# Performance work log

Measured on AMD Instinct MI355X. Metric: run time of the kernel, lower is better.

## Reference

```python
import jax, jax.numpy as jnp
import numpy as np

EPS = 1e-6      # F.pairwise_distance adds eps to the difference vector
MARGIN = 0.2
NORM_EPS = 1e-12  # torch F.normalize clamps the norm at 1e-12


def _l2_normalize(x):
    n = jnp.linalg.norm(x, axis=1, keepdims=True)
    return x / jnp.maximum(n, NORM_EPS)


def _pairdist(A, B):
    # ||a - b + EPS||_2 for every (a, b) pair, computed without the [N,N,d] tensor:
    # ||a-b||^2 + 2*EPS*sum(a-b) + d*EPS^2
    d = A.shape[1]
    sq = (jnp.sum(A * A, axis=1)[:, None] + jnp.sum(B * B, axis=1)[None, :]
          - 2.0 * (A @ B.T)
          + 2.0 * EPS * (jnp.sum(A, axis=1)[:, None] - jnp.sum(B, axis=1)[None, :])
          + d * (EPS * EPS))
    return jnp.sqrt(jnp.maximum(sq, 0.0))


def setup_inputs() -> dict:
    key = jax.random.key(0)
    kp, kn = jax.random.split(key)
    p = jax.random.normal(kp, (8192, 128), dtype=jnp.float32)
    n = jax.random.normal(kn, (64, 128), dtype=jnp.float32)
    return {"sequence_representations_p": p, "sequence_representations_n": n}


def reference(sequence_representations_p, sequence_representations_n):
    p = _l2_normalize(sequence_representations_p)  # [l_p, d]
    n = _l2_normalize(sequence_representations_n)  # [l_n, d]
    l_p = p.shape[0]
    t = 0  # original uses random.randint(0, l_n-1); fixed for determinism
    d_pp = _pairdist(p, p)                 # [l_p, l_p]
    d_pn = _pairdist(p, n[t:t + 1])[:, 0]  # [l_p]
    distance = jnp.maximum(d_pp + MARGIN - d_pn[:, None], 0.0)
    loss = jnp.sum(distance) / ((l_p - 1) * l_p)
    return jnp.maximum(loss, 0.0)
```

## Files before the change

kernel.cpp:

```cpp
#include <hip/hip_runtime.h>
#include <hip/hip_bf16.h>

typedef float f32x16 __attribute__((ext_vector_type(16)));
typedef float f32x4v __attribute__((ext_vector_type(4)));

#define GLOBAL_AS(p) ((const __attribute__((address_space(1))) void*)(p))
#define LDS_AS(p)    ((__attribute__((address_space(3))) void*)(p))

#define LP 8192
#define D 128
#define TWOEPS 2e-6f
#define CEPS 1.28e-10f
#define MARGIN 0.2f
#define NTRI 2080
#define NBLK 512
#define INV_DENOM 1.4903545e-8f

#define BUFSZ 34816
#define AOFF 0
#define BOFF 16384
#define QWOFF 32768

__global__ __launch_bounds__(64) void rows_kernel(const float* __restrict__ p,
                                                  const float* __restrict__ n,
                                                  char* __restrict__ pb,
                                                  float* __restrict__ qw) {
    const int lane = threadIdx.x;
    const int sub = lane & 3;
    const int r = lane >> 2;
    const int row = blockIdx.x * 16 + r;

    const float4* px = (const float4*)(p + (size_t)row * D + sub * 32);
    const float4* nx = (const float4*)(n + sub * 32);
    float4 x[8], y[8];
#pragma unroll
    for (int k = 0; k < 8; ++k) { x[k] = px[k]; y[k] = nx[k]; }

    float ssp = 0.0f, ssn = 0.0f;
#pragma unroll
    for (int k = 0; k < 8; ++k) {
        ssp += fmaf(x[k].x, x[k].x, fmaf(x[k].y, x[k].y,
               fmaf(x[k].z, x[k].z, x[k].w * x[k].w)));
        ssn += fmaf(y[k].x, y[k].x, fmaf(y[k].y, y[k].y,
               fmaf(y[k].z, y[k].z, y[k].w * y[k].w)));
    }
    ssp += __shfl_xor(ssp, 1); ssp += __shfl_xor(ssp, 2);
    ssn += __shfl_xor(ssn, 1); ssn += __shfl_xor(ssn, 2);

    const float invp = 1.0f / fmaxf(sqrtf(ssp), 1e-12f);
    const float invn = 1.0f / fmaxf(sqrtf(ssn), 1e-12f);

    float s = 0.0f, q = 0.0f, dn = 0.0f, sn = 0.0f, qn = 0.0f, q8 = 0.0f;
    int pk8[8];
#pragma unroll
    for (int k = 0; k < 8; ++k) {
        float a0 = x[k].x * invp, a1 = x[k].y * invp,
              a2 = x[k].z * invp, a3 = x[k].w * invp;
        float h0 = y[k].x * invn, h1 = y[k].y * invn,
              h2 = y[k].z * invn, h3 = y[k].w * invn;
        s  += (a0 + a1) + (a2 + a3);
        q  += fmaf(a0, a0, fmaf(a1, a1, fmaf(a2, a2, a3 * a3)));
        dn += fmaf(a0, h0, fmaf(a1, h1, fmaf(a2, h2, a3 * h3)));
        sn += (h0 + h1) + (h2 + h3);
        qn += fmaf(h0, h0, fmaf(h1, h1, fmaf(h2, h2, h3 * h3)));
        int wlo = __builtin_amdgcn_cvt_pk_fp8_f32(a0, a1, 0, false);
        int wfl = __builtin_amdgcn_cvt_pk_fp8_f32(a2, a3, wlo, true);
        pk8[k] = wfl;
        float b0 = __builtin_amdgcn_cvt_f32_fp8(wfl, 0);
        float b1 = __builtin_amdgcn_cvt_f32_fp8(wfl, 1);
        float b2 = __builtin_amdgcn_cvt_f32_fp8(wfl, 2);
        float b3 = __builtin_amdgcn_cvt_f32_fp8(wfl, 3);
        q8 += fmaf(b0, b0, fmaf(b1, b1, fmaf(b2, b2, b3 * b3)));
    }
    char* dst = pb + (size_t)row * 128 + sub * 32;
    ((int4*)dst)[0] = make_int4(pk8[0], pk8[1], pk8[2], pk8[3]);
    ((int4*)dst)[1] = make_int4(pk8[4], pk8[5], pk8[6], pk8[7]);

#pragma unroll
    for (int m = 1; m < 4; m <<= 1) {
        s += __shfl_xor(s, m);
        q += __shfl_xor(q, m);
        dn += __shfl_xor(dn, m);
        sn += __shfl_xor(sn, m);
        qn += __shfl_xor(qn, m);
        q8 += __shfl_xor(q8, m);
    }
    if (sub == 0) {
        float sq = q + qn - 2.0f * dn + TWOEPS * (s - sn) + CEPS;
        float dpn = sqrtf(fmaxf(sq, 0.0f));
        *(float2*)(qw + (size_t)row * 2) = make_float2(q8, MARGIN - dpn);
    }
}

__global__ __launch_bounds__(512, 4) void pair_kernel(const char* __restrict__ pb,
                                                      const float* __restrict__ qw,
                                                      float* __restrict__ out) {
    __shared__ __align__(16) char smem[2 * BUFSZ];
    const int blk = blockIdx.x;
    const int tid = threadIdx.x;
    const int wave = tid >> 6, lane = tid & 63;
    const int nt = (blk < NTRI - 4 * NBLK) ? 5 : 4;

    const int wr = wave >> 2, wc = wave & 3;
    const int ln31 = lane & 31;
    const int h = lane >> 5;

    auto decode = [](int b, int& ti, int& tj) {
        int t = (int)((__builtin_amdgcn_sqrtf(8.0f * (float)b + 1.0f) - 1.0f) * 0.5f);
        while ((t + 1) * (t + 2) / 2 <= b) ++t;
        while (t * (t + 1) / 2 > b) --t;
        ti = t;
        tj = b - t * (t + 1) / 2;
    };

    auto stage = [&](int ti, int tj, char* buf) {
        const char* gA = pb + (size_t)ti * 128 * 128;
        const char* gB = pb + (size_t)tj * 128 * 128;
#pragma unroll
        for (int r = 0; r < 2; ++r) {
            int obase = wave * 2048 + r * 1024;
            int o = obase + lane * 16;
            int src = o ^ (((o >> 7) & 7) << 4);
            __builtin_amdgcn_global_load_lds(GLOBAL_AS(gA + src),
                                             LDS_AS(buf + AOFF + obase), 16, 0, 0);
            __builtin_amdgcn_global_load_lds(GLOBAL_AS(gB + src),
                                             LDS_AS(buf + BOFF + obase), 16, 0, 0);
        }
        int side = wave >> 2;
        int chunk = wave & 3;
        const char* gq = (const char*)qw + (size_t)(side ? tj : ti) * 1024 +
                         chunk * 256 + lane * 4;
        __builtin_amdgcn_global_load_lds(GLOBAL_AS(gq),
                                         LDS_AS(buf + QWOFF + side * 1024 + chunk * 256),
                                         4, 0, 0);
    };

    int ti0, tj0;
    decode(blk, ti0, tj0);
    stage(ti0, tj0, smem);
    bool diag_cur = (ti0 == tj0);
    bool diag_nxt = false;

    float la0 = 0.0f, la1 = 0.0f, lb0 = 0.0f, lb1 = 0.0f;

    for (int t = 0; t < nt; ++t) {
        char* cur = smem + (size_t)(t & 1) * BUFSZ;
        char* nxt = smem + (size_t)((t + 1) & 1) * BUFSZ;

        if (t + 1 < nt) {
            int ti, tj;
            decode(blk + (t + 1) * NBLK, ti, tj);
            diag_nxt = (ti == tj);
            stage(ti, tj, nxt);
            asm volatile("s_waitcnt vmcnt(5)" ::: "memory");
        } else {
            asm volatile("s_waitcnt vmcnt(0)" ::: "memory");
        }
        __builtin_amdgcn_s_barrier();
        __builtin_amdgcn_sched_barrier(0);

        const char* lA = cur + AOFF;
        const char* lB = cur + BOFF;
        const float* qwi = (const float*)(cur + QWOFF);
        const float* qwj = (const float*)(cur + QWOFF + 1024);

        f32x16 acc[2] = {};
        __builtin_amdgcn_s_setprio(1);
#pragma unroll
        for (int ks = 0; ks < 8; ++ks) {
            int co = ((ks ^ (ln31 & 7)) << 4) + h * 8;
            long bv = *(const long*)(lB + (wc * 32 + ln31) * 128 + co);
#pragma unroll
            for (int mt = 0; mt < 2; ++mt) {
                long av = *(const long*)(lA + (wr * 64 + mt * 32 + ln31) * 128 + co);
                acc[mt] = __builtin_amdgcn_mfma_f32_32x32x16_fp8_fp8(av, bv, acc[mt],
                                                                     0, 0, 0);
            }
        }
        __builtin_amdgcn_s_setprio(0);

        float2 qwjv = *(const float2*)(qwj + (wc * 32 + ln31) * 2);
        if (diag_cur) {
#pragma unroll
            for (int mt = 0; mt < 2; ++mt)
#pragma unroll
                for (int g = 0; g < 4; ++g) {
                    int rbase = wr * 64 + mt * 32 + 8 * g + 4 * h;
                    f32x4v qw01 = *(const f32x4v*)(qwi + rbase * 2);
                    f32x4v qw23 = *(const f32x4v*)(qwi + rbase * 2 + 4);
                    float qi[4] = {qw01[0], qw01[2], qw23[0], qw23[2]};
                    float wi[4] = {qw01[1], qw01[3], qw23[1], qw23[3]};
#pragma unroll
                    for (int r2 = 0; r2 < 4; ++r2) {
                        float sq = fmaf(-2.0f, acc[mt][g * 4 + r2], qi[r2] + qwjv.x);
                        float d = __builtin_amdgcn_sqrtf(fmaxf(sq, 0.0f));
                        if (mt) la1 += fmaxf(d + wi[r2], 0.0f);
                        else    la0 += fmaxf(d + wi[r2], 0.0f);
                    }
                }
        } else {
#pragma unroll
            for (int mt = 0; mt < 2; ++mt)
#pragma unroll
                for (int g = 0; g < 4; ++g) {
                    int rbase = wr * 64 + mt * 32 + 8 * g + 4 * h;
                    f32x4v qw01 = *(const f32x4v*)(qwi + rbase * 2);
                    f32x4v qw23 = *(const f32x4v*)(qwi + rbase * 2 + 4);
                    float qi[4] = {qw01[0], qw01[2], qw23[0], qw23[2]};
                    float wi[4] = {qw01[1], qw01[3], qw23[1], qw23[3]};
#pragma unroll
                    for (int r2 = 0; r2 < 4; ++r2) {
                        float sq = fmaf(-2.0f, acc[mt][g * 4 + r2], qi[r2] + qwjv.x);
                        float d = __builtin_amdgcn_sqrtf(sq);
                        if (mt) { la1 += fmaxf(d + wi[r2], 0.0f);
                                  lb1 += fmaxf(d + qwjv.y, 0.0f); }
                        else    { la0 += fmaxf(d + wi[r2], 0.0f);
                                  lb0 += fmaxf(d + qwjv.y, 0.0f); }
                    }
                }
        }
        __builtin_amdgcn_s_barrier();
        diag_cur = diag_nxt;
    }

    float local = (la0 + la1) + (lb0 + lb1);
#pragma unroll
    for (int m = 1; m < 64; m <<= 1) local += __shfl_xor(local, m);
    float* sred = (float*)smem;
    if (lane == 0) sred[wave] = local;
    __syncthreads();
    if (tid == 0) {
        float t0 = (sred[0] + sred[1]) + (sred[2] + sred[3]);
        float t1 = (sred[4] + sred[5]) + (sred[6] + sred[7]);
        atomicAdd(out, (t0 + t1) * INV_DENOM);
    }
}

extern "C" void kernel_launch(void* const* d_in, const int* in_sizes, int n_in,
                              void* d_out, int out_size, void* d_ws, size_t ws_size,
                              hipStream_t stream) {
    const float* p = (const float*)d_in[0];
    const float* n = (const float*)d_in[1];
    float* out = (float*)d_out;
    char* ws = (char*)d_ws;

    char*  pb    = ws;
    float* qwarr = (float*)(ws + (1u << 20));

    hipMemsetAsync(out, 0, sizeof(float), stream);
    hipLaunchKernelGGL(rows_kernel, dim3(LP / 16), dim3(64), 0, stream, p, n, pb, qwarr);
    hipLaunchKernelGGL(pair_kernel, dim3(NBLK), dim3(512), 0, stream, pb, qwarr, out);
}
```

Before: 32.67 us.

## Replace static tile assignment with atomic work-stealing and register-staged LDS loads

The pair kernel now takes triangle tiles dynamically from a global atomic counter instead of a fixed stride assignment, to even out per-block load. Tile loads go through registers into a k-major LDS layout, where before they were direct global-to-LDS loads into a swizzled layout, so the next tile's global loads overlap the current MFMA work. The memset is folded into rows_kernel, and setprio is removed. Each tile now costs an extra atomic and a __syncthreads, and register pressure rises. The k-major layout may also cause LDS bank conflicts.

```diff
diff --git a/kernel.cpp b/kernel.cpp
--- a/kernel.cpp
+++ b/kernel.cpp
@@ -24,8 +24,11 @@
 __global__ __launch_bounds__(64) void rows_kernel(const float* __restrict__ p,
                                                   const float* __restrict__ n,
                                                   char* __restrict__ pb,
-                                                  float* __restrict__ qw) {
+                                                  float* __restrict__ qw,
+                                                  int* __restrict__ ctr,
+                                                  float* __restrict__ out) {
     const int lane = threadIdx.x;
+    if (blockIdx.x == 0 && lane == 0) { out[0] = 0.0f; ctr[0] = 0; }
     const int sub = lane & 3;
     const int r = lane >> 2;
     const int row = blockIdx.x * 16 + r;
@@ -94,13 +97,13 @@
 
 __global__ __launch_bounds__(512, 4) void pair_kernel(const char* __restrict__ pb,
                                                       const float* __restrict__ qw,
+                                                      int* __restrict__ ctr,
                                                       float* __restrict__ out) {
-    __shared__ __align__(16) char smem[2 * BUFSZ];
-    const int blk = blockIdx.x;
+    __shared__ __align__(16) char smem[2 * BUFSZ + 16];
+    int* slot = (int*)(smem + 2 * BUFSZ);
+
     const int tid = threadIdx.x;
     const int wave = tid >> 6, lane = tid & 63;
-    const int nt = (blk < NTRI - 4 * NBLK) ? 5 : 4;
-
     const int wr = wave >> 2, wc = wave & 3;
     const int ln31 = lane & 31;
     const int h = lane >> 5;
@@ -113,21 +116,18 @@
         tj = b - t * (t + 1) / 2;
     };
 
-    auto stage = [&](int ti, int tj, char* buf) {
-        const char* gA = pb + (size_t)ti * 128 * 128;
-        const char* gB = pb + (size_t)tj * 128 * 128;
+    auto issue = [&](int idx, char* buf, int4* ra, int4* rb) {
+        int ti, tj;
+        decode(idx, ti, tj);
+        const char* gA = pb + (size_t)ti * 16384;
+        const char* gB = pb + (size_t)tj * 16384;
 #pragma unroll
         for (int r = 0; r < 2; ++r) {
-            int obase = wave * 2048 + r * 1024;
-            int o = obase + lane * 16;
-            int src = o ^ (((o >> 7) & 7) << 4);
-            __builtin_amdgcn_global_load_lds(GLOBAL_AS(gA + src),
-                                             LDS_AS(buf + AOFF + obase), 16, 0, 0);
-            __builtin_amdgcn_global_load_lds(GLOBAL_AS(gB + src),
-                                             LDS_AS(buf + BOFF + obase), 16, 0, 0);
-        }
-        int side = wave >> 2;
-        int chunk = wave & 3;
+            int o = wave * 2048 + r * 1024 + lane * 16;
+            ra[r] = *(const int4*)(gA + o);
+            rb[r] = *(const int4*)(gB + o);
+        }
+        int side = wave >> 2, chunk = wave & 3;
         const char* gq = (const char*)qw + (size_t)(side ? tj : ti) * 1024 +
                          chunk * 256 + lane * 4;
         __builtin_amdgcn_global_load_lds(GLOBAL_AS(gq),
@@ -135,52 +135,63 @@
                                          4, 0, 0);
     };
 
-    int ti0, tj0;
-    decode(blk, ti0, tj0);
-    stage(ti0, tj0, smem);
-    bool diag_cur = (ti0 == tj0);
-    bool diag_nxt = false;
+    auto writep = [&](char* buf, int4* ra, int4* rb) {
+#pragma unroll
+        for (int r = 0; r < 2; ++r) {
+            int c = lane & 7;
+            int row = wave * 16 + r * 8 + (lane >> 3);
+            *(int4*)(buf + AOFF + c * 2048 + row * 16) = ra[r];
+            *(int4*)(buf + BOFF + c * 2048 + row * 16) = rb[r];
+        }
+    };
+
+    if (tid == 0) *slot = atomicAdd(ctr, 1);
+    __syncthreads();
+    int icur = *slot;
+    bool vcur = icur < NTRI;
+
+    int4 ra[2], rb[2];
+    if (vcur) {
+        issue(icur, smem, ra, rb);
+        writep(smem, ra, rb);
+    }
+    if (tid == 0) *slot = atomicAdd(ctr, 1);
+    __syncthreads();
+    int inxt = *slot;
 
     float la0 = 0.0f, la1 = 0.0f, lb0 = 0.0f, lb1 = 0.0f;
-
-    for (int t = 0; t < nt; ++t) {
-        char* cur = smem + (size_t)(t & 1) * BUFSZ;
-        char* nxt = smem + (size_t)((t + 1) & 1) * BUFSZ;
-
-        if (t + 1 < nt) {
-            int ti, tj;
-            decode(blk + (t + 1) * NBLK, ti, tj);
-            diag_nxt = (ti == tj);
-            stage(ti, tj, nxt);
-            asm volatile("s_waitcnt vmcnt(5)" ::: "memory");
-        } else {
-            asm volatile("s_waitcnt vmcnt(0)" ::: "memory");
-        }
-        __builtin_amdgcn_s_barrier();
-        __builtin_amdgcn_sched_barrier(0);
-
-        const char* lA = cur + AOFF;
-        const char* lB = cur + BOFF;
-        const float* qwi = (const float*)(cur + QWOFF);
-        const float* qwj = (const float*)(cur + QWOFF + 1024);
+    int cur = 0;
+
+    while (vcur) {
+        char* bufc = smem + (size_t)cur * BUFSZ;
+        char* bufn = smem + (size_t)(cur ^ 1) * BUFSZ;
+        bool vnxt = inxt < NTRI;
+        if (vnxt) issue(inxt, bufn, ra, rb);
+
+        int ti, tj;
+        decode(icur, ti, tj);
+        const bool diag = (ti == tj);
+
+        const char* lA = bufc + AOFF;
+        const char* lB = bufc + BOFF;
+        const float* qwi = (const float*)(bufc + QWOFF);
+        const float* qwj = (const float*)(bufc + QWOFF + 1024);
 
         f32x16 acc[2] = {};
-        __builtin_amdgcn_s_setprio(1);
 #pragma unroll
         for (int ks = 0; ks < 8; ++ks) {
-            int co = ((ks ^ (ln31 & 7)) << 4) + h * 8;
-            long bv = *(const long*)(lB + (wc * 32 + ln31) * 128 + co);
+            int ko = ks * 2048 + h * 8;
+            long bv = *(const long*)(lB + ko + (wc * 32 + ln31) * 16);
 #pragma unroll
             for (int mt = 0; mt < 2; ++mt) {
-                long av = *(const long*)(lA + (wr * 64 + mt * 32 + ln31) * 128 + co);
+                long av = *(const long*)(lA + ko + (wr * 64 + mt * 32 + ln31) * 16);
                 acc[mt] = __builtin_amdgcn_mfma_f32_32x32x16_fp8_fp8(av, bv, acc[mt],
                                                                      0, 0, 0);
             }
         }
-        __builtin_amdgcn_s_setprio(0);
 
         float2 qwjv = *(const float2*)(qwj + (wc * 32 + ln31) * 2);
-        if (diag_cur) {
+        if (diag) {
 #pragma unroll
             for (int mt = 0; mt < 2; ++mt)
 #pragma unroll
@@ -219,8 +230,14 @@
                     }
                 }
         }
-        __builtin_amdgcn_s_barrier();
-        diag_cur = diag_nxt;
+
+        if (vnxt) writep(bufn, ra, rb);
+        if (tid == 0) *slot = atomicAdd(ctr, 1);
+        __syncthreads();
+        icur = inxt;
+        vcur = vnxt;
+        inxt = *slot;
+        cur ^= 1;
     }
 
     float local = (la0 + la1) + (lb0 + lb1);
@@ -246,8 +263,9 @@
 
     char*  pb    = ws;
     float* qwarr = (float*)(ws + (1u << 20));
-
-    hipMemsetAsync(out, 0, sizeof(float), stream);
-    hipLaunchKernelGGL(rows_kernel, dim3(LP / 16), dim3(64), 0, stream, p, n, pb, qwarr);
-    hipLaunchKernelGGL(pair_kernel, dim3(NBLK), dim3(512), 0, stream, pb, qwarr, out);
+    int*   ctr   = (int*)(ws + (1u << 20) + (64u << 10));
+
+    hipLaunchKernelGGL(rows_kernel, dim3(LP / 16), dim3(64), 0, stream, p, n, pb, qwarr,
+                       ctr, out);
+    hipLaunchKernelGGL(pair_kernel, dim3(NBLK), dim3(512), 0, stream, pb, qwarr, ctr, out);
 }
```

Result: slower. 50.29 us (+54.0%).

## Assign consecutive triangle tiles per block to reuse A tile and drop memset

Applied to the files above, without the earlier changes.

Replaces the strided triangular tile assignment with contiguous runs of tiles, laid out as paired triangle rows of 65 tiles, so consecutive iterations usually share the same A row-tile. The A tile and its per-row norm and margin values are then reloaded only when the row changes, and only the B tile plus its norm values are streamed each step. The output zeroing moves from a separate hipMemsetAsync into the rows kernel, removing one launch. LDS layout and the wait counts become conditional on whether A changes, which adds bookkeeping and makes the pipelining more complex.

```diff
diff --git a/kernel.cpp b/kernel.cpp
--- a/kernel.cpp
+++ b/kernel.cpp
@@ -16,16 +16,20 @@
 #define NBLK 512
 #define INV_DENOM 1.4903545e-8f
 
-#define BUFSZ 34816
-#define AOFF 0
-#define BOFF 16384
-#define QWOFF 32768
+#define TILEB 16384
+#define BQ (TILEB + 1024)
+#define A0OFF 0
+#define A1OFF 16384
+#define B0OFF 32768
+#define B1OFF (32768 + BQ)
 
 __global__ __launch_bounds__(64) void rows_kernel(const float* __restrict__ p,
                                                   const float* __restrict__ n,
                                                   char* __restrict__ pb,
-                                                  float* __restrict__ qw) {
+                                                  float* __restrict__ qw,
+                                                  float* __restrict__ out) {
     const int lane = threadIdx.x;
+    if (blockIdx.x == 0 && lane == 0) out[0] = 0.0f;
     const int sub = lane & 3;
     const int r = lane >> 2;
     const int row = blockIdx.x * 16 + r;
@@ -95,137 +99,137 @@
 __global__ __launch_bounds__(512, 4) void pair_kernel(const char* __restrict__ pb,
                                                       const float* __restrict__ qw,
                                                       float* __restrict__ out) {
-    __shared__ __align__(16) char smem[2 * BUFSZ];
-    const int blk = blockIdx.x;
+    __shared__ __align__(16) char smem[2 * TILEB + 2 * BQ];
     const int tid = threadIdx.x;
     const int wave = tid >> 6, lane = tid & 63;
-    const int nt = (blk < NTRI - 4 * NBLK) ? 5 : 4;
-
     const int wr = wave >> 2, wc = wave & 3;
     const int ln31 = lane & 31;
     const int h = lane >> 5;
-
-    auto decode = [](int b, int& ti, int& tj) {
-        int t = (int)((__builtin_amdgcn_sqrtf(8.0f * (float)b + 1.0f) - 1.0f) * 0.5f);
-        while ((t + 1) * (t + 2) / 2 <= b) ++t;
-        while (t * (t + 1) / 2 > b) --t;
-        ti = t;
-        tj = b - t * (t + 1) / 2;
+    const int blk = blockIdx.x;
+
+    const int g0 = blk * 4 + (blk < 32 ? blk : 32);
+    const int nt = (blk < 32) ? 5 : 4;
+
+    auto decode = [](int g, int& ti, int& tj) {
+        int s = g / 65;
+        int pos = g - s * 65;
+        if (pos <= s) { ti = s; tj = pos; }
+        else          { ti = 63 - s; tj = pos - s - 1; }
     };
 
-    auto stage = [&](int ti, int tj, char* buf) {
-        const char* gA = pb + (size_t)ti * 128 * 128;
-        const char* gB = pb + (size_t)tj * 128 * 128;
+    auto stageT = [&](int tt, char* buf) {
 #pragma unroll
         for (int r = 0; r < 2; ++r) {
-            int obase = wave * 2048 + r * 1024;
-            int o = obase + lane * 16;
-            int src = o ^ (((o >> 7) & 7) << 4);
-            __builtin_amdgcn_global_load_lds(GLOBAL_AS(gA + src),
-                                             LDS_AS(buf + AOFF + obase), 16, 0, 0);
-            __builtin_amdgcn_global_load_lds(GLOBAL_AS(gB + src),
-                                             LDS_AS(buf + BOFF + obase), 16, 0, 0);
-        }
-        int side = wave >> 2;
-        int chunk = wave & 3;
-        const char* gq = (const char*)qw + (size_t)(side ? tj : ti) * 1024 +
-                         chunk * 256 + lane * 4;
-        __builtin_amdgcn_global_load_lds(GLOBAL_AS(gq),
-                                         LDS_AS(buf + QWOFF + side * 1024 + chunk * 256),
-                                         4, 0, 0);
+            int o = wave * 2048 + r * 1024;
+            int ol = o + lane * 16;
+            int src = ol ^ (((ol >> 7) & 7) << 4);
+            __builtin_amdgcn_global_load_lds(GLOBAL_AS(pb + (size_t)tt * TILEB + src),
+                                             LDS_AS(buf + o), 16, 0, 0);
+        }
     };
+    auto stageQ = [&](int tj, char* buf) {
+        if (lane < 32)
+            __builtin_amdgcn_global_load_lds(
+                GLOBAL_AS((const char*)qw + (size_t)tj * 1024 + wave * 128 + lane * 4),
+                LDS_AS(buf + TILEB + wave * 128), 4, 0, 0);
+    };
 
     int ti0, tj0;
-    decode(blk, ti0, tj0);
-    stage(ti0, tj0, smem);
-    bool diag_cur = (ti0 == tj0);
-    bool diag_nxt = false;
-
+    decode(g0, ti0, tj0);
+    stageT(ti0, smem + A0OFF);
+    stageT(tj0, smem + B0OFF);
+    stageQ(tj0, smem + B0OFF);
+    int apar = 0;
+    int tiLoaded = -1;
+    float qi[2][4][4], wi[2][4][4];
     float la0 = 0.0f, la1 = 0.0f, lb0 = 0.0f, lb1 = 0.0f;
 
     for (int t = 0; t < nt; ++t) {
-        char* cur = smem + (size_t)(t & 1) * BUFSZ;
-        char* nxt = smem + (size_t)((t + 1) & 1) * BUFSZ;
-
+        int ti, tj;
+        decode(g0 + t, ti, tj);
+        bool chA = false;
         if (t + 1 < nt) {
-            int ti, tj;
-            decode(blk + (t + 1) * NBLK, ti, tj);
-            diag_nxt = (ti == tj);
-            stage(ti, tj, nxt);
-            asm volatile("s_waitcnt vmcnt(5)" ::: "memory");
+            int ti1, tj1;
+            decode(g0 + t + 1, ti1, tj1);
+            chA = (ti1 != ti);
+            char* bn = smem + (((t + 1) & 1) ? B1OFF : B0OFF);
+            stageT(tj1, bn);
+            stageQ(tj1, bn);
+            if (chA) {
+                stageT(ti1, smem + ((apar ^ 1) ? A1OFF : A0OFF));
+                asm volatile("s_waitcnt vmcnt(5)" ::: "memory");
+            } else {
+                asm volatile("s_waitcnt vmcnt(3)" ::: "memory");
+            }
         } else {
             asm volatile("s_waitcnt vmcnt(0)" ::: "memory");
         }
         __builtin_amdgcn_s_barrier();
         __builtin_amdgcn_sched_barrier(0);
 
-        const char* lA = cur + AOFF;
-        const char* lB = cur + BOFF;
-        const float* qwi = (const float*)(cur + QWOFF);
-        const float* qwj = (const float*)(cur + QWOFF + 1024);
-
-        f32x16 acc[2] = {};
-        __builtin_amdgcn_s_setprio(1);
+        if (ti != tiLoaded) {
+            tiLoaded = ti;
+            const float* qwi = qw + (size_t)ti * 256;
+#pragma unroll
+            for (int mt = 0; mt < 2; ++mt)
+#pragma unroll
+                for (int g = 0; g < 4; ++g) {
+                    int rbase = wr * 64 + mt * 32 + 8 * g + 4 * h;
+                    f32x4v a = *(const f32x4v*)(qwi + rbase * 2);
+                    f32x4v b = *(const f32x4v*)(qwi + rbase * 2 + 4);
+                    qi[mt][g][0] = a[0]; wi[mt][g][0] = a[1];
+                    qi[mt][g][1] = a[2]; wi[mt][g][1] = a[3];
+                    qi[mt][g][2] = b[0]; wi[mt][g][2] = b[1];
+                    qi[mt][g][3] = b[2]; wi[mt][g][3] = b[3];
+                }
+        }
+
+        const char* lA = smem + (apar ? A1OFF : A0OFF);
+        const char* lB = smem + ((t & 1) ? B1OFF : B0OFF);
+
+        f32x16 acc0 = {}, acc1 = {};
 #pragma unroll
         for (int ks = 0; ks < 8; ++ks) {
             int co = ((ks ^ (ln31 & 7)) << 4) + h * 8;
-            long bv = *(const long*)(lB + (wc * 32 + ln31) * 128 + co);
-#pragma unroll
-            for (int mt = 0; mt < 2; ++mt) {
-                long av = *(const long*)(lA + (wr * 64 + mt * 32 + ln31) * 128 + co);
-                acc[mt] = __builtin_amdgcn_mfma_f32_32x32x16_fp8_fp8(av, bv, acc[mt],
-                                                                     0, 0, 0);
+            long bv  = *(const long*)(lB + (wc * 32 + ln31) * 128 + co);
+            long av0 = *(const long*)(lA + (wr * 64 + ln31) * 128 + co);
+            long av1 = *(const long*)(lA + (wr * 64 + 32 + ln31) * 128 + co);
+            acc0 = __builtin_amdgcn_mfma_f32_32x32x16_fp8_fp8(av0, bv, acc0, 0, 0, 0);
+            acc1 = __builtin_amdgcn_mfma_f32_32x32x16_fp8_fp8(av1, bv, acc1, 0, 0, 0);
+        }
+
+        float2 qwjv = *(const float2*)(lB + TILEB + (wc * 32 + ln31) * 8);
+        const bool diag = (ti == tj);
+#pragma unroll
+        for (int g = 0; g < 4; ++g)
+#pragma unroll
+            for (int r2 = 0; r2 < 4; ++r2) {
+                float sq0 = fmaf(-2.0f, acc0[g * 4 + r2], qi[0][g][r2] + qwjv.x);
+                float sq1 = fmaf(-2.0f, acc1[g * 4 + r2], qi[1][g][r2] + qwjv.x);
+                if (diag) {
+                    float d0 = __builtin_amdgcn_sqrtf(fmaxf(sq0, 0.0f));
+                    float d1 = __builtin_amdgcn_sqrtf(fmaxf(sq1, 0.0f));
+                    la0 += fmaxf(d0 + wi[0][g][r2], 0.0f);
+                    la1 += fmaxf(d1 + wi[1][g][r2], 0.0f);
+                } else {
+                    float d0 = __builtin_amdgcn_sqrtf(sq0);
+                    float d1 = __builtin_amdgcn_sqrtf(sq1);
+                    la0 += fmaxf(d0 + wi[0][g][r2], 0.0f);
+                    la1 += fmaxf(d1 + wi[1][g][r2], 0.0f);
+                    lb0 += fmaxf(d0 + qwjv.y, 0.0f);
+                    lb1 += fmaxf(d1 + qwjv.y, 0.0f);
+                }
             }
-        }
-        __builtin_amdgcn_s_setprio(0);
-
-        float2 qwjv = *(const float2*)(qwj + (wc * 32 + ln31) * 2);
-        if (diag_cur) {
-#pragma unroll
-            for (int mt = 0; mt < 2; ++mt)
-#pragma unroll
-                for (int g = 0; g < 4; ++g) {
-                    int rbase = wr * 64 + mt * 32 + 8 * g + 4 * h;
-                    f32x4v qw01 = *(const f32x4v*)(qwi + rbase * 2);
-                    f32x4v qw23 = *(const f32x4v*)(qwi + rbase * 2 + 4);
-                    float qi[4] = {qw01[0], qw01[2], qw23[0], qw23[2]};
-                    float wi[4] = {qw01[1], qw01[3], qw23[1], qw23[3]};
-#pragma unroll
-                    for (int r2 = 0; r2 < 4; ++r2) {
-                        float sq = fmaf(-2.0f, acc[mt][g * 4 + r2], qi[r2] + qwjv.x);
-                        float d = __builtin_amdgcn_sqrtf(fmaxf(sq, 0.0f));
-                        if (mt) la1 += fmaxf(d + wi[r2], 0.0f);
-                        else    la0 += fmaxf(d + wi[r2], 0.0f);
-                    }
-                }
-        } else {
-#pragma unroll
-            for (int mt = 0; mt < 2; ++mt)
-#pragma unroll
-                for (int g = 0; g < 4; ++g) {
-                    int rbase = wr * 64 + mt * 32 + 8 * g + 4 * h;
-                    f32x4v qw01 = *(const f32x4v*)(qwi + rbase * 2);
-                    f32x4v qw23 = *(const f32x4v*)(qwi + rbase * 2 + 4);
-                    float qi[4] = {qw01[0], qw01[2], qw23[0], qw23[2]};
-                    float wi[4] = {qw01[1], qw01[3], qw23[1], qw23[3]};
-#pragma unroll
-                    for (int r2 = 0; r2 < 4; ++r2) {
-                        float sq = fmaf(-2.0f, acc[mt][g * 4 + r2], qi[r2] + qwjv.x);
-                        float d = __builtin_amdgcn_sqrtf(sq);
-                        if (mt) { la1 += fmaxf(d + wi[r2], 0.0f);
-                                  lb1 += fmaxf(d + qwjv.y, 0.0f); }
-                        else    { la0 += fmaxf(d + wi[r2], 0.0f);
-                                  lb0 += fmaxf(d + qwjv.y, 0.0f); }
-                    }
-                }
-        }
+
+        __builtin_amdgcn_sched_barrier(0);
         __builtin_amdgcn_s_barrier();
-        diag_cur = diag_nxt;
+        if (chA) apar ^= 1;
     }
 
     float local = (la0 + la1) + (lb0 + lb1);
 #pragma unroll
     for (int m = 1; m < 64; m <<= 1) local += __shfl_xor(local, m);
+    __syncthreads();
     float* sred = (float*)smem;
     if (lane == 0) sred[wave] = local;
     __syncthreads();
@@ -247,7 +251,7 @@
     char*  pb    = ws;
     float* qwarr = (float*)(ws + (1u << 20));
 
-    hipMemsetAsync(out, 0, sizeof(float), stream);
-    hipLaunchKernelGGL(rows_kernel, dim3(LP / 16), dim3(64), 0, stream, p, n, pb, qwarr);
+    hipLaunchKernelGGL(rows_kernel, dim3(LP / 16), dim3(64), 0, stream, p, n, pb, qwarr,
+                       out);
     hipLaunchKernelGGL(pair_kernel, dim3(NBLK), dim3(512), 0, stream, pb, qwarr, out);
 }
```

Measured after the change: 33.26 us. No clear change (+1.8%).

## Use 128x64 tiles with register-resident A fragments and triple-buffered B staging

Applied to the files above, without the earlier changes.

Replaces the 128x128 triangular tiling with 128x64 tiles grouped so each block walks consecutive B tiles of the same A row-tile. The A fragment is kept in registers and reloaded only when the row tile changes, while B is streamed through a three-slot LDS ring. Per-row scalars now come straight from global memory instead of being staged in LDS. The output memset is folded into the first kernel and the grid doubles to 1024 blocks with a higher occupancy target. This trades extra global loads and smaller MFMA reuse per tile for less LDS traffic and a lower launch overhead.

```diff
diff --git a/kernel.cpp b/kernel.cpp
--- a/kernel.cpp
+++ b/kernel.cpp
@@ -12,20 +12,19 @@
 #define TWOEPS 2e-6f
 #define CEPS 1.28e-10f
 #define MARGIN 0.2f
-#define NTRI 2080
-#define NBLK 512
+#define NTILE 4160
+#define NBLK 1024
 #define INV_DENOM 1.4903545e-8f
-
-#define BUFSZ 34816
-#define AOFF 0
-#define BOFF 16384
-#define QWOFF 32768
+#define BTILE 8192
 
 __global__ __launch_bounds__(64) void rows_kernel(const float* __restrict__ p,
                                                   const float* __restrict__ n,
                                                   char* __restrict__ pb,
-                                                  float* __restrict__ qw) {
+                                                  float* __restrict__ qarr,
+                                                  float* __restrict__ warr,
+                                                  float* __restrict__ out) {
     const int lane = threadIdx.x;
+    if (blockIdx.x == 0 && lane == 0) out[0] = 0.0f;
     const int sub = lane & 3;
     const int r = lane >> 2;
     const int row = blockIdx.x * 16 + r;
@@ -88,144 +87,107 @@
     if (sub == 0) {
         float sq = q + qn - 2.0f * dn + TWOEPS * (s - sn) + CEPS;
         float dpn = sqrtf(fmaxf(sq, 0.0f));
-        *(float2*)(qw + (size_t)row * 2) = make_float2(q8, MARGIN - dpn);
+        qarr[row] = q8;
+        warr[row] = MARGIN - dpn;
     }
 }
 
-__global__ __launch_bounds__(512, 4) void pair_kernel(const char* __restrict__ pb,
-                                                      const float* __restrict__ qw,
+__global__ __launch_bounds__(512, 8) void pair_kernel(const char* __restrict__ pb,
+                                                      const float* __restrict__ qarr,
+                                                      const float* __restrict__ warr,
                                                       float* __restrict__ out) {
-    __shared__ __align__(16) char smem[2 * BUFSZ];
-    const int blk = blockIdx.x;
+    __shared__ __align__(16) char smem[3 * BTILE + 64];
     const int tid = threadIdx.x;
     const int wave = tid >> 6, lane = tid & 63;
-    const int nt = (blk < NTRI - 4 * NBLK) ? 5 : 4;
-
-    const int wr = wave >> 2, wc = wave & 3;
+    const int wavei = wave >> 1, wavej = wave & 1;
     const int ln31 = lane & 31;
     const int h = lane >> 5;
-
-    auto decode = [](int b, int& ti, int& tj) {
-        int t = (int)((__builtin_amdgcn_sqrtf(8.0f * (float)b + 1.0f) - 1.0f) * 0.5f);
-        while ((t + 1) * (t + 2) / 2 <= b) ++t;
-        while (t * (t + 1) / 2 > b) --t;
-        ti = t;
-        tj = b - t * (t + 1) / 2;
+    const int blk = blockIdx.x;
+
+    const int g0 = (blk < 64) ? 5 * blk : 320 + 4 * (blk - 64);
+    const int nt = (blk < 64) ? 5 : 4;
+
+    auto decode = [](int g, int& I, int& J) {
+        int t = (int)((__builtin_amdgcn_sqrtf(4.0f * (float)g + 1.0f) - 1.0f) * 0.5f);
+        while ((t + 1) * (t + 2) <= g) ++t;
+        while (t * (t + 1) > g) --t;
+        I = t;
+        J = g - t * (t + 1);
     };
 
-    auto stage = [&](int ti, int tj, char* buf) {
-        const char* gA = pb + (size_t)ti * 128 * 128;
-        const char* gB = pb + (size_t)tj * 128 * 128;
-#pragma unroll
-        for (int r = 0; r < 2; ++r) {
-            int obase = wave * 2048 + r * 1024;
-            int o = obase + lane * 16;
-            int src = o ^ (((o >> 7) & 7) << 4);
-            __builtin_amdgcn_global_load_lds(GLOBAL_AS(gA + src),
-                                             LDS_AS(buf + AOFF + obase), 16, 0, 0);
-            __builtin_amdgcn_global_load_lds(GLOBAL_AS(gB + src),
-                                             LDS_AS(buf + BOFF + obase), 16, 0, 0);
-        }
-        int side = wave >> 2;
-        int chunk = wave & 3;
-        const char* gq = (const char*)qw + (size_t)(side ? tj : ti) * 1024 +
-                         chunk * 256 + lane * 4;
-        __builtin_amdgcn_global_load_lds(GLOBAL_AS(gq),
-                                         LDS_AS(buf + QWOFF + side * 1024 + chunk * 256),
-                                         4, 0, 0);
+    auto stage = [&](int g, int slot) {
+        int I, J;
+        decode(g, I, J);
+        const char* gB = pb + (size_t)J * BTILE;
+        int o = wave * 1024 + lane * 16;
+        int src = o ^ (((o >> 7) & 7) << 4);
+        __builtin_amdgcn_global_load_lds(GLOBAL_AS(gB + src),
+                                         LDS_AS(smem + slot * BTILE + wave * 1024),
+                                         16, 0, 0);
     };
 
-    int ti0, tj0;
-    decode(blk, ti0, tj0);
-    stage(ti0, tj0, smem);
-    bool diag_cur = (ti0 == tj0);
-    bool diag_nxt = false;
-
-    float la0 = 0.0f, la1 = 0.0f, lb0 = 0.0f, lb1 = 0.0f;
+    stage(g0, 0);
+    if (nt > 1) stage(g0 + 1, 1);
+
+    int curI = -1;
+    long afr[8];
+    float la = 0.0f, lb = 0.0f;
 
     for (int t = 0; t < nt; ++t) {
-        char* cur = smem + (size_t)(t & 1) * BUFSZ;
-        char* nxt = smem + (size_t)((t + 1) & 1) * BUFSZ;
-
-        if (t + 1 < nt) {
-            int ti, tj;
-            decode(blk + (t + 1) * NBLK, ti, tj);
-            diag_nxt = (ti == tj);
-            stage(ti, tj, nxt);
-            asm volatile("s_waitcnt vmcnt(5)" ::: "memory");
-        } else {
-            asm volatile("s_waitcnt vmcnt(0)" ::: "memory");
-        }
+        int I, J;
+        decode(g0 + t, I, J);
+
+        if (t + 1 < nt) asm volatile("s_waitcnt vmcnt(1)" ::: "memory");
+        else            asm volatile("s_waitcnt vmcnt(0)" ::: "memory");
         __builtin_amdgcn_s_barrier();
         __builtin_amdgcn_sched_barrier(0);
 
-        const char* lA = cur + AOFF;
-        const char* lB = cur + BOFF;
-        const float* qwi = (const float*)(cur + QWOFF);
-        const float* qwj = (const float*)(cur + QWOFF + 1024);
-
-        f32x16 acc[2] = {};
-        __builtin_amdgcn_s_setprio(1);
+        if (I != curI) {
+            curI = I;
+            const char* gA = pb + (size_t)I * 16384 + (wavei * 32 + ln31) * 128 + h * 8;
+#pragma unroll
+            for (int ks = 0; ks < 8; ++ks) afr[ks] = *(const long*)(gA + ks * 16);
+        }
+        const int j = J * 64 + wavej * 32 + ln31;
+        const float qj = qarr[j];
+        const float wj = warr[j];
+
+        if (t + 2 < nt) stage(g0 + t + 2, (t + 2) % 3);
+
+        const char* lB = smem + (size_t)(t % 3) * BTILE;
+        f32x16 acc = {};
 #pragma unroll
         for (int ks = 0; ks < 8; ++ks) {
             int co = ((ks ^ (ln31 & 7)) << 4) + h * 8;
-            long bv = *(const long*)(lB + (wc * 32 + ln31) * 128 + co);
-#pragma unroll
-            for (int mt = 0; mt < 2; ++mt) {
-                long av = *(const long*)(lA + (wr * 64 + mt * 32 + ln31) * 128 + co);
-                acc[mt] = __builtin_amdgcn_mfma_f32_32x32x16_fp8_fp8(av, bv, acc[mt],
-                                                                     0, 0, 0);
+            long bv = *(const long*)(lB + (wavej * 32 + ln31) * 128 + co);
+            acc = __builtin_amdgcn_mfma_f32_32x32x16_fp8_fp8(afr[ks], bv, acc, 0, 0, 0);
+        }
+
+        const bool dtype = ((J >> 1) == I);
+#pragma unroll
+        for (int gg = 0; gg < 4; ++gg) {
+            int rbase = I * 128 + wavei * 32 + 8 * gg + 4 * h;
+            f32x4v q4 = *(const f32x4v*)(qarr + rbase);
+            f32x4v w4 = *(const f32x4v*)(warr + rbase);
+#pragma unroll
+            for (int r2 = 0; r2 < 4; ++r2) {
+                float sq = fmaf(-2.0f, acc[gg * 4 + r2], q4[r2] + qj);
+                if (dtype) {
+                    float d = __builtin_amdgcn_sqrtf(fmaxf(sq, 0.0f));
+                    la += fmaxf(d + w4[r2], 0.0f);
+                } else {
+                    float d = __builtin_amdgcn_sqrtf(sq);
+                    la += fmaxf(d + w4[r2], 0.0f);
+                    lb += fmaxf(d + wj, 0.0f);
+                }
             }
         }
-        __builtin_amdgcn_s_setprio(0);
-
-        float2 qwjv = *(const float2*)(qwj + (wc * 32 + ln31) * 2);
-        if (diag_cur) {
-#pragma unroll
-            for (int mt = 0; mt < 2; ++mt)
-#pragma unroll
-                for (int g = 0; g < 4; ++g) {
-                    int rbase = wr * 64 + mt * 32 + 8 * g + 4 * h;
-                    f32x4v qw01 = *(const f32x4v*)(qwi + rbase * 2);
-                    f32x4v qw23 = *(const f32x4v*)(qwi + rbase * 2 + 4);
-                    float qi[4] = {qw01[0], qw01[2], qw23[0], qw23[2]};
-                    float wi[4] = {qw01[1], qw01[3], qw23[1], qw23[3]};
-#pragma unroll
-                    for (int r2 = 0; r2 < 4; ++r2) {
-                        float sq = fmaf(-2.0f, acc[mt][g * 4 + r2], qi[r2] + qwjv.x);
-                        float d = __builtin_amdgcn_sqrtf(fmaxf(sq, 0.0f));
-                        if (mt) la1 += fmaxf(d + wi[r2], 0.0f);
-                        else    la0 += fmaxf(d + wi[r2], 0.0f);
-                    }
-                }
-        } else {
-#pragma unroll
-            for (int mt = 0; mt < 2; ++mt)
-#pragma unroll
-                for (int g = 0; g < 4; ++g) {
-                    int rbase = wr * 64 + mt * 32 + 8 * g + 4 * h;
-                    f32x4v qw01 = *(const f32x4v*)(qwi + rbase * 2);
-                    f32x4v qw23 = *(const f32x4v*)(qwi + rbase * 2 + 4);
-                    float qi[4] = {qw01[0], qw01[2], qw23[0], qw23[2]};
-                    float wi[4] = {qw01[1], qw01[3], qw23[1], qw23[3]};
-#pragma unroll
-                    for (int r2 = 0; r2 < 4; ++r2) {
-                        float sq = fmaf(-2.0f, acc[mt][g * 4 + r2], qi[r2] + qwjv.x);
-                        float d = __builtin_amdgcn_sqrtf(sq);
-                        if (mt) { la1 += fmaxf(d + wi[r2], 0.0f);
-                                  lb1 += fmaxf(d + qwjv.y, 0.0f); }
-                        else    { la0 += fmaxf(d + wi[r2], 0.0f);
-                                  lb0 += fmaxf(d + qwjv.y, 0.0f); }
-                    }
-                }
-        }
-        __builtin_amdgcn_s_barrier();
-        diag_cur = diag_nxt;
-    }
-
-    float local = (la0 + la1) + (lb0 + lb1);
+    }
+
+    float local = la + lb;
 #pragma unroll
     for (int m = 1; m < 64; m <<= 1) local += __shfl_xor(local, m);
+    __syncthreads();
     float* sred = (float*)smem;
     if (lane == 0) sred[wave] = local;
     __syncthreads();
@@ -245,9 +207,10 @@
     char* ws = (char*)d_ws;
 
     char*  pb    = ws;
-    float* qwarr = (float*)(ws + (1u << 20));
-
-    hipMemsetAsync(out, 0, sizeof(float), stream);
-    hipLaunchKernelGGL(rows_kernel, dim3(LP / 16), dim3(64), 0, stream, p, n, pb, qwarr);
-    hipLaunchKernelGGL(pair_kernel, dim3(NBLK), dim3(512), 0, stream, pb, qwarr, out);
+    float* qarr  = (float*)(ws + (1u << 20));
+    float* warr  = (float*)(ws + (1u << 20) + (32u << 10));
+
+    hipLaunchKernelGGL(rows_kernel, dim3(LP / 16), dim3(64), 0, stream, p, n, pb,
+                       qarr, warr, out);
+    hipLaunchKernelGGL(pair_kernel, dim3(NBLK), dim3(512), 0, stream, pb, qarr, warr, out);
 }
```

Measured after the change: 39.25 us. 1.2x slower.
